# Performance work log

Measured on AMD Instinct MI355X. Metric: run time of the kernel, lower is better.

## Reference

```python
import jax, jax.numpy as jnp
import numpy as np


def _maxpool2x2(x):
    # x: [N, C, H, W] -> [N, C, H//2, W//2]
    N, C, H, W = x.shape
    x = x.reshape(N, C, H // 2, 2, W // 2, 2)
    return x.max(axis=(3, 5))


def setup_inputs() -> dict:
    key = jax.random.key(0)
    ks = jax.random.split(key, 6)
    N, C, H, W = 16, 64, 64, 64
    x = jax.random.normal(ks[0], (N, C, H, W), dtype=jnp.float32)
    # 1x1 conv weights, stored as [out_ch, in_ch] (kernel is 1x1, no bias)
    w_theta = jax.random.normal(ks[1], (C >> 3, C), dtype=jnp.float32) * 0.05
    w_phi = jax.random.normal(ks[2], (C >> 3, C), dtype=jnp.float32) * 0.05
    w_g = jax.random.normal(ks[3], (C >> 1, C), dtype=jnp.float32) * 0.05
    w_o = jax.random.normal(ks[4], (C, C >> 1), dtype=jnp.float32) * 0.05
    gamma = jax.random.normal(ks[5], (), dtype=jnp.float32)
    return {"x": x, "w_theta": w_theta, "w_phi": w_phi, "w_g": w_g, "w_o": w_o, "gamma": gamma}


def reference(x, w_theta, w_phi, w_g, w_o, gamma):
    N, C, H, W = x.shape
    L = H * W           # location_num
    D = L >> 2          # downsampled_num
    # 1x1 convs as channel contractions
    theta = jnp.einsum('oc,nchw->nohw', w_theta, x).reshape(N, C >> 3, L)
    phi = _maxpool2x2(jnp.einsum('oc,nchw->nohw', w_phi, x)).reshape(N, C >> 3, D)
    attn = jax.nn.softmax(jnp.einsum('nkl,nkd->nld', theta, phi), axis=-1)  # [N, L, D]
    g = _maxpool2x2(jnp.einsum('oc,nchw->nohw', w_g, x)).reshape(N, C >> 1, D)
    attn_g = jnp.einsum('ngd,nld->ngl', g, attn).reshape(N, C >> 1, H, W)
    attn_g = jnp.einsum('og,nghw->nohw', w_o, attn_g)
    return x + gamma * attn_g
```

## Files before the change

kernel.cpp:

```cpp
#include <hip/hip_runtime.h>
#include <hip/hip_bf16.h>
#include <hip/hip_fp16.h>

#define NB 16
#define CCH 64
#define LL 4096
#define DD 1024

typedef _Float16 h8 __attribute__((ext_vector_type(8)));
typedef _Float16 h2 __attribute__((ext_vector_type(2)));
typedef float    f4v __attribute__((ext_vector_type(4)));

#if defined(__has_builtin)
#if __has_builtin(__builtin_amdgcn_fdot2)
#define HAVE_FDOT2 1
#endif
#if __has_builtin(__builtin_amdgcn_exp2f)
#define EXP2F(x) __builtin_amdgcn_exp2f(x)
#endif
#endif
#ifndef EXP2F
#define EXP2F(x) exp2f(x)
#endif

static __device__ __forceinline__ float fdot2f(h2 a, h2 b, float c) {
#ifdef HAVE_FDOT2
    return __builtin_amdgcn_fdot2(a, b, c, false);
#else
    return c + (float)a[0] * (float)b[0] + (float)a[1] * (float)b[1];
#endif
}

#define MFMA16(a, b, c) __builtin_amdgcn_mfma_f32_16x16x32_f16((a), (b), (c), 0, 0, 0)

__global__ __launch_bounds__(256, 6) void prep_kernel(
    const float* __restrict__ x,
    const float* __restrict__ w_theta,
    const float* __restrict__ w_phi,
    const float* __restrict__ w_g,
    _Float16* __restrict__ theta_out,
    _Float16* __restrict__ phi_out,
    _Float16* __restrict__ gT_out)
{
    __shared__ __align__(16) float smem[64 * 68];
    float* xs   = smem;
    float* pool = smem;

    const int n    = blockIdx.x >> 6;
    const int rem  = blockIdx.x & 63;
    const int rg   = rem >> 1;
    const int half = rem & 1;
    const int tid  = threadIdx.x;
    const int w    = tid >> 6;
    const int lane = tid & 63;
    const int m16  = lane & 15;
    const int quad = lane >> 4;

    h8 bf[3][2];
#pragma unroll
    for (int t = 0; t < 3; ++t) {
        const float* row;
        float scale = 1.0f;
        if (t == 0) {
            if (m16 < 8) { row = w_theta + m16 * 64; scale = 1.44269504f; }
            else         { row = w_phi + (m16 - 8) * 64; }
        } else if (t == 1) {
            row = w_g + m16 * 64;
        } else {
            row = w_g + (16 + m16) * 64;
        }
#pragma unroll
        for (int kc = 0; kc < 2; ++kc) {
            const float* p = row + kc * 32 + quad * 8;
            float4 a = *(const float4*)p;
            float4 b = *(const float4*)(p + 4);
            bf[t][kc][0] = (_Float16)(a.x * scale);
            bf[t][kc][1] = (_Float16)(a.y * scale);
            bf[t][kc][2] = (_Float16)(a.z * scale);
            bf[t][kc][3] = (_Float16)(a.w * scale);
            bf[t][kc][4] = (_Float16)(b.x * scale);
            bf[t][kc][5] = (_Float16)(b.y * scale);
            bf[t][kc][6] = (_Float16)(b.z * scale);
            bf[t][kc][7] = (_Float16)(b.w * scale);
        }
    }

    {
        const int ch = tid >> 2;
        const int s  = tid & 3;
        const float* xc = x + (size_t)n * CCH * LL + (size_t)ch * LL;
        float4 vv[4];
#pragma unroll
        for (int i = 0; i < 4; ++i) {
            const int f    = i * 4 + s;
            const int row  = f >> 3;
            const int colg = f & 7;
            const int l    = (rg * 2 + row) * 64 + half * 32 + colg * 4;
            vv[i] = *(const float4*)(xc + l);
        }
#pragma unroll
        for (int i = 0; i < 4; ++i) {
            const int f    = i * 4 + s;
            const int row  = f >> 3;
            const int colg = f & 7;
            *(float4*)(xs + ch * 68 + row * 32 + colg * 4) = vv[i];
        }
    }
    __syncthreads();

    h8 af[2];
#pragma unroll
    for (int kc = 0; kc < 2; ++kc) {
#pragma unroll
        for (int j = 0; j < 8; ++j) {
            float v = xs[(kc * 32 + quad * 8 + j) * 68 + w * 16 + m16];
            af[kc][j] = (_Float16)v;
        }
    }

    f4v cfr[3];
#pragma unroll
    for (int t = 0; t < 3; ++t) {
        f4v c = {0.f, 0.f, 0.f, 0.f};
        c = MFMA16(af[0], bf[t][0], c);
        c = MFMA16(af[1], bf[t][1], c);
        cfr[t] = c;
    }
    __syncthreads();

    {
#pragma unroll
        for (int t = 0; t < 3; ++t) {
#pragma unroll
            for (int r = 0; r < 4; ++r)
                pool[(w * 16 + quad * 4 + r) * 49 + t * 16 + m16] = cfr[t][r];
        }
    }
    __syncthreads();

    if (tid < 64) {
        const int px  = tid;
        const int row = px >> 5, col = px & 31;
        const int l   = (rg * 2 + row) * 64 + half * 32 + col;
        const float* pr = pool + px * 49;
        h8 tv;
#pragma unroll
        for (int k = 0; k < 8; ++k) tv[k] = (_Float16)pr[k];
        *(h8*)(theta_out + ((size_t)n * LL + l) * 8) = tv;
    }

    const int d_base = rg * 32 + half * 16;
    for (int idx = tid; idx < 640; idx += 256) {
        const int f40 = idx >> 4;
        const int pc  = idx & 15;
        const int fcol = 8 + f40;
        float v = fmaxf(fmaxf(pool[(2 * pc) * 49 + fcol],      pool[(2 * pc + 1) * 49 + fcol]),
                        fmaxf(pool[(32 + 2 * pc) * 49 + fcol], pool[(33 + 2 * pc) * 49 + fcol]));
        const int d = d_base + pc;
        if (f40 < 8) phi_out[((size_t)n * DD + d) * 8 + f40] = (_Float16)v;
        else         gT_out[((size_t)n * 32 + (f40 - 8)) * DD + d] = (_Float16)v;
    }
}

__global__ __launch_bounds__(256, 8) void attn_kernel(
    const float*    __restrict__ x,
    const _Float16* __restrict__ theta,
    const _Float16* __restrict__ phi,
    const _Float16* __restrict__ gT,
    const float*    __restrict__ w_o,
    const float*    __restrict__ gamma_p,
    float*          __restrict__ out)
{
    __shared__ __align__(16) char smem[18944 + 512];
    _Float16* phi_s  = (_Float16*)smem;
    float*    red    = (float*)smem;
    float*    out_s  = (float*)smem;
    float*    ssum_s = (float*)(smem + 18944);

    const int n    = blockIdx.x >> 7;
    const int lblk = blockIdx.x & 127;
    const int tid  = threadIdx.x;
    const int h    = tid >> 6;
    const int lane = tid & 63;
    const int m16  = lane & 15;
    const int quad = lane >> 4;
    const int l0   = lblk * 32;

    const _Float16* gT_n = gT + (size_t)n * 32 * DD;

    {
        const float4* ps = (const float4*)(phi + (size_t)n * DD * 8);
        float4* pd = (float4*)phi_s;
#pragma unroll
        for (int i = 0; i < 4; ++i) {
            const int d = tid + 256 * i;
            pd[d + (d >> 3)] = ps[d];
        }
    }

    h8 th0 = *(const h8*)(theta + ((size_t)n * LL + l0 + m16) * 8);
    h8 th1 = *(const h8*)(theta + ((size_t)n * LL + l0 + 16 + m16) * 8);
    const h2* t0p = (const h2*)&th0;
    const h2* t1p = (const h2*)&th1;

    const int vp = h >> 1;
    h8 wof[2];
#pragma unroll
    for (int i = 0; i < 2; ++i) {
        const float* wr = w_o + (size_t)(m16 + 16 * (vp * 2 + i)) * 32 + quad * 8;
        float4 wa = *(const float4*)wr;
        float4 wb = *(const float4*)(wr + 4);
        wof[i][0] = (_Float16)wa.x; wof[i][1] = (_Float16)wa.y;
        wof[i][2] = (_Float16)wa.z; wof[i][3] = (_Float16)wa.w;
        wof[i][4] = (_Float16)wb.x; wof[i][5] = (_Float16)wb.y;
        wof[i][6] = (_Float16)wb.z; wof[i][7] = (_Float16)wb.w;
    }

    __syncthreads();

    f4v c00 = {0.f, 0.f, 0.f, 0.f}, c01 = c00, c10 = c00, c11 = c00;
    float ssum0 = 0.f, ssum1 = 0.f;

    const _Float16* gr0 = gT_n + (size_t)m16 * DD + h * 256 + quad * 8;
    const _Float16* gr1 = gT_n + (size_t)(16 + m16) * DD + h * 256 + quad * 8;
    const int pb = h * 256 + quad * 8;
    const _Float16* pr = phi_s + (size_t)(pb + (pb >> 3)) * 8;

#pragma unroll 2
    for (int c = 0; c < 8; ++c) {
        const int d0 = c * 32;
        h8 b0 = *(const h8*)(gr0 + d0);
        h8 b1 = *(const h8*)(gr1 + d0);
        const _Float16* prc = pr + c * 288;
        h8 a0, a1;
#pragma unroll
        for (int j = 0; j < 8; ++j) {
            h8 ph = *(const h8*)(prc + j * 8);
            const h2* pp = (const h2*)&ph;
            float u0 = fdot2f(t0p[0], pp[0], 0.f);
            u0 = fdot2f(t0p[1], pp[1], u0);
            float v0 = fdot2f(t0p[2], pp[2], 0.f);
            v0 = fdot2f(t0p[3], pp[3], v0);
            float u1 = fdot2f(t1p[0], pp[0], 0.f);
            u1 = fdot2f(t1p[1], pp[1], u1);
            float v1 = fdot2f(t1p[2], pp[2], 0.f);
            v1 = fdot2f(t1p[3], pp[3], v1);
            float e0 = EXP2F(u0 + v0);
            float e1 = EXP2F(u1 + v1);
            ssum0 += e0; ssum1 += e1;
            a0[j] = (_Float16)e0;
            a1[j] = (_Float16)e1;
        }
        c00 = MFMA16(a0, b0, c00);
        c01 = MFMA16(a0, b1, c01);
        c10 = MFMA16(a1, b0, c10);
        c11 = MFMA16(a1, b1, c11);
    }

    ssum0 += __shfl_xor(ssum0, 16); ssum0 += __shfl_xor(ssum0, 32);
    ssum1 += __shfl_xor(ssum1, 16); ssum1 += __shfl_xor(ssum1, 32);
    if (quad == 0) {
        ssum_s[h * 32 + m16]      = ssum0;
        ssum_s[h * 32 + 16 + m16] = ssum1;
    }
    __syncthreads();

    {
        float* rg = red + (size_t)h * 32 * 37;
#pragma unroll
        for (int r = 0; r < 4; ++r) {
            const int rr = quad * 4 + r;
            rg[rr * 37 + m16]             = c00[r];
            rg[rr * 37 + 16 + m16]        = c01[r];
            rg[(16 + rr) * 37 + m16]      = c10[r];
            rg[(16 + rr) * 37 + 16 + m16] = c11[r];
        }
    }
    __syncthreads();

    const int t = h & 1;
    h8 pa;
    {
        const int q = t * 16 + m16;
        const float* rq = red + q * 37 + quad * 8;
        float ss = ssum_s[q] + ssum_s[32 + q] + ssum_s[64 + q] + ssum_s[96 + q];
        float inv = 1.0f / ss;
#pragma unroll
        for (int j = 0; j < 8; ++j) {
            float sv = rq[j] + rq[32 * 37 + j] + rq[64 * 37 + j] + rq[96 * 37 + j];
            pa[j] = (_Float16)(sv * inv);
        }
    }
    __syncthreads();

    const f4v zero = {0.f, 0.f, 0.f, 0.f};
#pragma unroll
    for (int i = 0; i < 2; ++i) {
        f4v pv = MFMA16(pa, wof[i], zero);
        const int och = m16 + 16 * (vp * 2 + i);
        float* od = out_s + (size_t)(t * 16 + quad * 4) * 68 + och;
#pragma unroll
        for (int r = 0; r < 4; ++r) od[r * 68] = pv[r];
    }
    __syncthreads();

    const float gamma = gamma_p[0];
    const int soch = tid >> 2;
    const int qoff = (tid & 3) * 8;
    const float* xrow = x   + (size_t)n * CCH * LL + (size_t)soch * LL + l0 + qoff;
    float*       orow = out + (size_t)n * CCH * LL + (size_t)soch * LL + l0 + qoff;
#pragma unroll
    for (int i = 0; i < 2; ++i) {
        float4 xv = *(const float4*)(xrow + i * 4);
        float4 ov;
        ov.x = xv.x + gamma * out_s[(qoff + i * 4)     * 68 + soch];
        ov.y = xv.y + gamma * out_s[(qoff + i * 4 + 1) * 68 + soch];
        ov.z = xv.z + gamma * out_s[(qoff + i * 4 + 2) * 68 + soch];
        ov.w = xv.w + gamma * out_s[(qoff + i * 4 + 3) * 68 + soch];
        *(float4*)(orow + i * 4) = ov;
    }
}

extern "C" void kernel_launch(void* const* d_in, const int* in_sizes, int n_in,
                              void* d_out, int out_size, void* d_ws, size_t ws_size,
                              hipStream_t stream) {
    const float* x       = (const float*)d_in[0];
    const float* w_theta = (const float*)d_in[1];
    const float* w_phi   = (const float*)d_in[2];
    const float* w_g     = (const float*)d_in[3];
    const float* w_o     = (const float*)d_in[4];
    const float* gamma   = (const float*)d_in[5];
    float* out = (float*)d_out;

    _Float16* theta_h = (_Float16*)d_ws;
    _Float16* phi_h   = theta_h + (size_t)NB * LL * 8;
    _Float16* gT_h    = phi_h   + (size_t)NB * DD * 8;

    prep_kernel<<<1024, 256, 0, stream>>>(x, w_theta, w_phi, w_g,
                                          theta_h, phi_h, gT_h);
    attn_kernel<<<2048, 256, 0, stream>>>(x, theta_h, phi_h, gT_h,
                                          w_o, gamma, out);
}
```

Measured before the change: 113.6 us.

## Compute attention scores with MFMA instead of fdot2 and permute gT layout

The theta·phi score products move from per-lane fdot2 VALU chains onto 16x16x32 f16 MFMAs. The K dimension is zero-padded from 8 to 32, so only quad-0 lanes load theta and phi. The exponentiated scores are written through a per-wave LDS buffer to re-shape them into MFMA A operands, and the prep kernel stores gT with a permuted d ordering to match that column layout. Shared-memory staging of phi is dropped in favour of direct global loads, row sums are reduced with lane shuffles, and occupancy bounds drop from 8 to 6. This trades most of the VALU work for wasted MFMA K-lanes and an extra LDS round trip per chunk.

Result: slower. 123.3 us (+8.5%).

```diff
diff --git a/kernel.cpp b/kernel.cpp
--- a/kernel.cpp
+++ b/kernel.cpp
@@ -12,9 +12,6 @@
 typedef float    f4v __attribute__((ext_vector_type(4)));
 
 #if defined(__has_builtin)
-#if __has_builtin(__builtin_amdgcn_fdot2)
-#define HAVE_FDOT2 1
-#endif
 #if __has_builtin(__builtin_amdgcn_exp2f)
 #define EXP2F(x) __builtin_amdgcn_exp2f(x)
 #endif
@@ -22,14 +19,6 @@
 #ifndef EXP2F
 #define EXP2F(x) exp2f(x)
 #endif
-
-static __device__ __forceinline__ float fdot2f(h2 a, h2 b, float c) {
-#ifdef HAVE_FDOT2
-    return __builtin_amdgcn_fdot2(a, b, c, false);
-#else
-    return c + (float)a[0] * (float)b[0] + (float)a[1] * (float)b[1];
-#endif
-}
 
 #define MFMA16(a, b, c) __builtin_amdgcn_mfma_f32_16x16x32_f16((a), (b), (c), 0, 0, 0)
 
@@ -156,13 +145,15 @@
         const int fcol = 8 + f40;
         float v = fmaxf(fmaxf(pool[(2 * pc) * 49 + fcol],      pool[(2 * pc + 1) * 49 + fcol]),
                         fmaxf(pool[(32 + 2 * pc) * 49 + fcol], pool[(33 + 2 * pc) * 49 + fcol]));
-        const int d = d_base + pc;
-        if (f40 < 8) phi_out[((size_t)n * DD + d) * 8 + f40] = (_Float16)v;
-        else         gT_out[((size_t)n * 32 + (f40 - 8)) * DD + d] = (_Float16)v;
+        if (f40 < 8) {
+            phi_out[((size_t)n * DD + d_base + pc) * 8 + f40] = (_Float16)v;
+        } else {
+            gT_out[((size_t)n * 32 + (f40 - 8)) * DD + rg * 32 + pc * 2 + half] = (_Float16)v;
+        }
     }
 }
 
-__global__ __launch_bounds__(256, 8) void attn_kernel(
+__global__ __launch_bounds__(256, 6) void attn_kernel(
     const float*    __restrict__ x,
     const _Float16* __restrict__ theta,
     const _Float16* __restrict__ phi,
@@ -172,7 +163,7 @@
     float*          __restrict__ out)
 {
     __shared__ __align__(16) char smem[18944 + 512];
-    _Float16* phi_s  = (_Float16*)smem;
+    _Float16* Pbuf   = (_Float16*)smem;
     float*    red    = (float*)smem;
     float*    out_s  = (float*)smem;
     float*    ssum_s = (float*)(smem + 18944);
@@ -186,22 +177,106 @@
     const int quad = lane >> 4;
     const int l0   = lblk * 32;
 
-    const _Float16* gT_n = gT + (size_t)n * 32 * DD;
+    const _Float16* gT_n  = gT  + (size_t)n * 32 * DD;
+    const _Float16* phi_n = phi + (size_t)n * DD * 8;
+    _Float16* Pw = Pbuf + h * 1280;
+
+    h8 th0 = {}, th1 = {};
+    if (quad == 0) {
+        th0 = *(const h8*)(theta + ((size_t)n * LL + l0 + m16) * 8);
+        th1 = *(const h8*)(theta + ((size_t)n * LL + l0 + 16 + m16) * 8);
+    }
+
+    const _Float16* gr0 = gT_n + (size_t)m16 * DD + h * 256 + quad * 8;
+    const _Float16* gr1 = gT_n + (size_t)(16 + m16) * DD + h * 256 + quad * 8;
+
+    f4v c00 = {0.f, 0.f, 0.f, 0.f}, c01 = c00, c10 = c00, c11 = c00;
+    float ss[2][4] = {{0.f, 0.f, 0.f, 0.f}, {0.f, 0.f, 0.f, 0.f}};
+    const f4v zero = {0.f, 0.f, 0.f, 0.f};
+
+#pragma unroll 2
+    for (int c = 0; c < 8; ++c) {
+        const int d0 = h * 256 + c * 32;
+        h8 b0 = *(const h8*)(gr0 + c * 32);
+        h8 b1 = *(const h8*)(gr1 + c * 32);
+        h8 bp0 = {}, bp1 = {};
+        if (quad == 0) {
+            bp0 = *(const h8*)(phi_n + (size_t)(d0 + m16) * 8);
+            bp1 = *(const h8*)(phi_n + (size_t)(d0 + 16 + m16) * 8);
+        }
+        f4v s00 = MFMA16(th0, bp0, zero);
+        f4v s10 = MFMA16(th1, bp0, zero);
+        f4v s01 = MFMA16(th0, bp1, zero);
+        f4v s11 = MFMA16(th1, bp1, zero);
+#pragma unroll
+        for (int r = 0; r < 4; ++r) {
+            float e00 = EXP2F(s00[r]);
+            float e01 = EXP2F(s01[r]);
+            ss[0][r] += e00 + e01;
+            h2 t0; t0[0] = (_Float16)e00; t0[1] = (_Float16)e01;
+            *(h2*)(Pw + (quad * 4 + r) * 40 + m16 * 2) = t0;
+            float e10 = EXP2F(s10[r]);
+            float e11 = EXP2F(s11[r]);
+            ss[1][r] += e10 + e11;
+            h2 t1; t1[0] = (_Float16)e10; t1[1] = (_Float16)e11;
+            *(h2*)(Pw + (16 + quad * 4 + r) * 40 + m16 * 2) = t1;
+        }
+        h8 pa0 = *(const h8*)(Pw + m16 * 40 + quad * 8);
+        h8 pa1 = *(const h8*)(Pw + (16 + m16) * 40 + quad * 8);
+        c00 = MFMA16(pa0, b0, c00);
+        c01 = MFMA16(pa0, b1, c01);
+        c10 = MFMA16(pa1, b0, c10);
+        c11 = MFMA16(pa1, b1, c11);
+    }
+
+#pragma unroll
+    for (int qt = 0; qt < 2; ++qt) {
+#pragma unroll
+        for (int r = 0; r < 4; ++r) {
+            float v = ss[qt][r];
+            v += __shfl_xor(v, 1);
+            v += __shfl_xor(v, 2);
+            v += __shfl_xor(v, 4);
+            v += __shfl_xor(v, 8);
+            ss[qt][r] = v;
+        }
+    }
+    if (m16 == 0) {
+#pragma unroll
+        for (int qt = 0; qt < 2; ++qt)
+#pragma unroll
+            for (int r = 0; r < 4; ++r)
+                ssum_s[h * 32 + qt * 16 + quad * 4 + r] = ss[qt][r];
+    }
+    __syncthreads();
 
     {
-        const float4* ps = (const float4*)(phi + (size_t)n * DD * 8);
-        float4* pd = (float4*)phi_s;
-#pragma unroll
-        for (int i = 0; i < 4; ++i) {
-            const int d = tid + 256 * i;
-            pd[d + (d >> 3)] = ps[d];
-        }
-    }
-
-    h8 th0 = *(const h8*)(theta + ((size_t)n * LL + l0 + m16) * 8);
-    h8 th1 = *(const h8*)(theta + ((size_t)n * LL + l0 + 16 + m16) * 8);
-    const h2* t0p = (const h2*)&th0;
-    const h2* t1p = (const h2*)&th1;
+        float* rg = red + (size_t)h * 32 * 37;
+#pragma unroll
+        for (int r = 0; r < 4; ++r) {
+            const int rr = quad * 4 + r;
+            rg[rr * 37 + m16]             = c00[r];
+            rg[rr * 37 + 16 + m16]        = c01[r];
+            rg[(16 + rr) * 37 + m16]      = c10[r];
+            rg[(16 + rr) * 37 + 16 + m16] = c11[r];
+        }
+    }
+    __syncthreads();
+
+    const int t = h & 1;
+    h8 pa;
+    {
+        const int q = t * 16 + m16;
+        const float* rq = red + q * 37 + quad * 8;
+        float sden = ssum_s[q] + ssum_s[32 + q] + ssum_s[64 + q] + ssum_s[96 + q];
+        float inv = 1.0f / sden;
+#pragma unroll
+        for (int j = 0; j < 8; ++j) {
+            float sv = rq[j] + rq[32 * 37 + j] + rq[64 * 37 + j] + rq[96 * 37 + j];
+            pa[j] = (_Float16)(sv * inv);
+        }
+    }
+    __syncthreads();
 
     const int vp = h >> 1;
     h8 wof[2];
@@ -216,84 +291,6 @@
         wof[i][6] = (_Float16)wb.z; wof[i][7] = (_Float16)wb.w;
     }
 
-    __syncthreads();
-
-    f4v c00 = {0.f, 0.f, 0.f, 0.f}, c01 = c00, c10 = c00, c11 = c00;
-    float ssum0 = 0.f, ssum1 = 0.f;
-
-    const _Float16* gr0 = gT_n + (size_t)m16 * DD + h * 256 + quad * 8;
-    const _Float16* gr1 = gT_n + (size_t)(16 + m16) * DD + h * 256 + quad * 8;
-    const int pb = h * 256 + quad * 8;
-    const _Float16* pr = phi_s + (size_t)(pb + (pb >> 3)) * 8;
-
-#pragma unroll 2
-    for (int c = 0; c < 8; ++c) {
-        const int d0 = c * 32;
-        h8 b0 = *(const h8*)(gr0 + d0);
-        h8 b1 = *(const h8*)(gr1 + d0);
-        const _Float16* prc = pr + c * 288;
-        h8 a0, a1;
-#pragma unroll
-        for (int j = 0; j < 8; ++j) {
-            h8 ph = *(const h8*)(prc + j * 8);
-            const h2* pp = (const h2*)&ph;
-            float u0 = fdot2f(t0p[0], pp[0], 0.f);
-            u0 = fdot2f(t0p[1], pp[1], u0);
-            float v0 = fdot2f(t0p[2], pp[2], 0.f);
-            v0 = fdot2f(t0p[3], pp[3], v0);
-            float u1 = fdot2f(t1p[0], pp[0], 0.f);
-            u1 = fdot2f(t1p[1], pp[1], u1);
-            float v1 = fdot2f(t1p[2], pp[2], 0.f);
-            v1 = fdot2f(t1p[3], pp[3], v1);
-            float e0 = EXP2F(u0 + v0);
-            float e1 = EXP2F(u1 + v1);
-            ssum0 += e0; ssum1 += e1;
-            a0[j] = (_Float16)e0;
-            a1[j] = (_Float16)e1;
-        }
-        c00 = MFMA16(a0, b0, c00);
-        c01 = MFMA16(a0, b1, c01);
-        c10 = MFMA16(a1, b0, c10);
-        c11 = MFMA16(a1, b1, c11);
-    }
-
-    ssum0 += __shfl_xor(ssum0, 16); ssum0 += __shfl_xor(ssum0, 32);
-    ssum1 += __shfl_xor(ssum1, 16); ssum1 += __shfl_xor(ssum1, 32);
-    if (quad == 0) {
-        ssum_s[h * 32 + m16]      = ssum0;
-        ssum_s[h * 32 + 16 + m16] = ssum1;
-    }
-    __syncthreads();
-
-    {
-        float* rg = red + (size_t)h * 32 * 37;
-#pragma unroll
-        for (int r = 0; r < 4; ++r) {
-            const int rr = quad * 4 + r;
-            rg[rr * 37 + m16]             = c00[r];
-            rg[rr * 37 + 16 + m16]        = c01[r];
-            rg[(16 + rr) * 37 + m16]      = c10[r];
-            rg[(16 + rr) * 37 + 16 + m16] = c11[r];
-        }
-    }
-    __syncthreads();
-
-    const int t = h & 1;
-    h8 pa;
-    {
-        const int q = t * 16 + m16;
-        const float* rq = red + q * 37 + quad * 8;
-        float ss = ssum_s[q] + ssum_s[32 + q] + ssum_s[64 + q] + ssum_s[96 + q];
-        float inv = 1.0f / ss;
-#pragma unroll
-        for (int j = 0; j < 8; ++j) {
-            float sv = rq[j] + rq[32 * 37 + j] + rq[64 * 37 + j] + rq[96 * 37 + j];
-            pa[j] = (_Float16)(sv * inv);
-        }
-    }
-    __syncthreads();
-
-    const f4v zero = {0.f, 0.f, 0.f, 0.f};
 #pragma unroll
     for (int i = 0; i < 2; ++i) {
         f4v pv = MFMA16(pa, wof[i], zero);
```
